# Kernel tuning notes

Hardware: AMD Instinct MI355X
Metric: run time of the kernel (lower is better)

The kernel has to match this reference:

```python
import jax, jax.numpy as jnp
import numpy as np
from jax import lax

B = 4096
D = 128
N = 81
H = 4
HD = D // H


def _conv(x, w, b, pad):
    y = lax.conv_general_dilated(x, w, (1, 1), [(pad, pad), (pad, pad)],
                                 dimension_numbers=('NCHW', 'OIHW', 'NCHW'))
    return y + b[None, :, None, None]


def _attn_mask():
    # per-head additive structural mask: same-row, same-col, same-box, global
    idx = jnp.arange(N)
    rows, cols = idx // 9, idx % 9
    boxes = rows // 3 * 3 + cols // 3
    same = lambda v: (v[:, None] == v[None, :]).astype(jnp.float32)
    return jnp.stack([same(rows), same(cols), same(boxes),
                      jnp.ones((N, N), jnp.float32)], 0)  # [4, 81, 81]


def setup_inputs():
    key = jax.random.key(0)
    ks = jax.random.split(key, 12)
    digits = jax.random.randint(ks[0], (B, 9, 9), 0, 10)
    s = jax.nn.one_hot(digits, 10, axis=1, dtype=jnp.float32)  # [B,10,9,9]

    def w(k, shape, fan):
        return jax.random.normal(k, shape, jnp.float32) / np.sqrt(fan)

    return {
        's': s,
        'c1_w': w(ks[1], (64, 10, 1, 1), 10), 'c1_b': jnp.zeros((64,)),
        'c2_w': w(ks[2], (128, 64, 3, 3), 64 * 9), 'c2_b': jnp.zeros((128,)),
        'c3_w': w(ks[3], (128, 128, 3, 3), 128 * 9), 'c3_b': jnp.zeros((128,)),
        'emb': 0.02 * jax.random.normal(ks[4], (1, N, D), jnp.float32),
        'in_w': w(ks[5], (3 * D, D), D), 'in_b': jnp.zeros((3 * D,)),
        'out_w': w(ks[6], (D, D), D), 'out_b': jnp.zeros((D,)),
        'ln_g': jnp.ones((D,)), 'ln_b': jnp.zeros((D,)),
        'l1_w': w(ks[7], (D, D), D), 'l1_b': jnp.zeros((D,)),
        'l2_w': w(ks[8], (D, D), D), 'l2_b': jnp.zeros((D,)),
        'pos_w': w(ks[9], (1, D), D), 'pos_b': jnp.zeros((1,)),
        'num_w': w(ks[10], (10, D), D), 'num_b': jnp.zeros((10,)),
    }


def reference(s, c1_w, c1_b, c2_w, c2_b, c3_w, c3_b, emb, in_w, in_b,
              out_w, out_b, ln_g, ln_b, l1_w, l1_b, l2_w, l2_b,
              pos_w, pos_b, num_w, num_b):
    # conv stem (note: no activation after c1, matching the torch code)
    x = _conv(s, c1_w, c1_b, 0)
    x = jax.nn.silu(_conv(x, c2_w, c2_b, 1))
    x = jax.nn.silu(_conv(x, c3_w, c3_b, 1))
    x = x.reshape(B, D, N).transpose(0, 2, 1) + emb  # [B,81,128]

    # MHA with per-head additive structural mask, no residual
    qkv = x @ in_w.T + in_b
    q, k, v = jnp.split(qkv, 3, axis=-1)
    heads = lambda t: t.reshape(B, N, H, HD).transpose(0, 2, 1, 3)
    q, k, v = heads(q), heads(k), heads(v)
    scores = jnp.einsum('bhqd,bhkd->bhqk', q, k) / np.sqrt(HD) + _attn_mask()[None]
    a = jax.nn.softmax(scores, axis=-1)          # [B,4,81,81]
    asc = a.mean(axis=1)                          # averaged attn weights
    ctx = jnp.einsum('bhqk,bhkd->bhqd', a, v).transpose(0, 2, 1, 3).reshape(B, N, D)
    x = ctx @ out_w.T + out_b

    # LayerNorm
    mu = x.mean(-1, keepdims=True)
    var = ((x - mu) ** 2).mean(-1, keepdims=True)
    x = (x - mu) / jnp.sqrt(var + 1e-5) * ln_g + ln_b

    x = jax.nn.silu(x @ l1_w.T + l1_b)
    x = jax.nn.silu(x @ l2_w.T + l2_b)

    # position head with masked softmax over empty cells
    pos_logits = (x @ pos_w.T + pos_b)[..., 0]    # [B,81]
    given = (s.argmax(1) != 0).reshape(B, N)
    pos_logits = jnp.where(given, -1e9, pos_logits)
    k1, k2 = jax.random.split(jax.random.key(42))
    pos = jax.random.categorical(k1, pos_logits)  # [B] int

    # number head at sampled position, digit 0 masked out
    num_logits = x @ num_w.T + num_b              # [B,81,10]
    o = jnp.take_along_axis(num_logits, pos[:, None, None], axis=1)[:, 0, :]
    o = o.at[:, 0].set(-jnp.inf)
    num = jax.random.categorical(k2, o)
    return pos, num, asc
```

## Files before the change

kernel.cpp:

```cpp
#include <hip/hip_runtime.h>
#include <stdint.h>
#include <math.h>


#define NB 4096

typedef unsigned short u16;
typedef _Float16 f16x8 __attribute__((ext_vector_type(8)));
typedef float f32x4 __attribute__((ext_vector_type(4)));

__device__ __forceinline__ float silu_f(float v) {
  return v / (1.0f + expf(-v));
}

__device__ __forceinline__ float4 zero4() { return make_float4(0.f,0.f,0.f,0.f); }

__device__ __forceinline__ void fma4b(float4& a, const float s, const float4 x) {
  a.x = fmaf(s, x.x, a.x); a.y = fmaf(s, x.y, a.y);
  a.z = fmaf(s, x.z, a.z); a.w = fmaf(s, x.w, a.w);
}

__device__ __forceinline__ void dacc(float& a, const float4 w, const float4 x) {
  a = fmaf(w.x, x.x, a); a = fmaf(w.y, x.y, a);
  a = fmaf(w.z, x.z, a); a = fmaf(w.w, x.w, a);
}

__device__ __forceinline__ void splitu(float v, u16& h, u16& l) {
  _Float16 hf = (_Float16)v;
  _Float16 lf = (_Float16)((v - (float)hf) * 2048.0f);
  union { _Float16 f; u16 u; } a, b;
  a.f = hf; b.f = lf;
  h = a.u; l = b.u;
}

__device__ __forceinline__ void tf_round(uint32_t& x0, uint32_t& x1, int r) {
  x0 += x1;
  x1 = (x1 << r) | (x1 >> (32 - r));
  x1 ^= x0;
}

__device__ __forceinline__ void threefry2x32(uint32_t k0, uint32_t k1,
                                             uint32_t x0, uint32_t x1,
                                             uint32_t& o0, uint32_t& o1) {
  uint32_t k2 = k0 ^ k1 ^ 0x1BD11BDAu;
  x0 += k0; x1 += k1;
  tf_round(x0,x1,13); tf_round(x0,x1,15); tf_round(x0,x1,26); tf_round(x0,x1,6);
  x0 += k1; x1 += k2 + 1u;
  tf_round(x0,x1,17); tf_round(x0,x1,29); tf_round(x0,x1,16); tf_round(x0,x1,24);
  x0 += k2; x1 += k0 + 2u;
  tf_round(x0,x1,13); tf_round(x0,x1,15); tf_round(x0,x1,26); tf_round(x0,x1,6);
  x0 += k0; x1 += k1 + 3u;
  tf_round(x0,x1,17); tf_round(x0,x1,29); tf_round(x0,x1,16); tf_round(x0,x1,24);
  x0 += k1; x1 += k2 + 4u;
  tf_round(x0,x1,13); tf_round(x0,x1,15); tf_round(x0,x1,26); tf_round(x0,x1,6);
  x0 += k2; x1 += k0 + 5u;
  o0 = x0; o1 = x1;
}

__device__ __forceinline__ void jax_split42(uint32_t& k1a, uint32_t& k1b,
                                            uint32_t& k2a, uint32_t& k2b) {
  threefry2x32(0u, 42u, 0u, 0u, k1a, k1b);
  threefry2x32(0u, 42u, 0u, 1u, k2a, k2b);
}

__device__ __forceinline__ uint32_t jax_randbits(uint32_t ka, uint32_t kb,
                                                 uint32_t i) {
  uint32_t o0, o1;
  threefry2x32(ka, kb, 0u, i, o0, o1);
  return o0 ^ o1;
}

__device__ __forceinline__ float jax_gumbel_bits(uint32_t bits) {
  float f = __uint_as_float((bits >> 9) | 0x3f800000u) - 1.0f;
  const float tiny = 1.17549435e-38f;
  float u = fmaxf(tiny, f + tiny);
  return -logf(-logf(u));
}

__global__ __launch_bounds__(256) void k_prep(
    const float* __restrict__ c1_w, const float* __restrict__ c1_b,
    const float* __restrict__ c2_w, const float* __restrict__ c3_w,
    const float* __restrict__ out_w, const float* __restrict__ l1_w,
    const float* __restrict__ l2_w,
    float* __restrict__ T2e, u16* __restrict__ WAh, u16* __restrict__ WAl,
    float* __restrict__ owT, float* __restrict__ l1T, float* __restrict__ l2T)
{
  int idx = blockIdx.x * 256 + threadIdx.x;
  if (idx < 9*11*128) {
    int oc = idx & 127;
    int t  = idx >> 7;
    int g  = t % 11;
    int d  = t / 11;
    float acc = 0.f;
    if (g < 10) {
      int di = d / 3, dj = d % 3;
      for (int ic = 0; ic < 64; ++ic) {
        float x1 = c1_w[ic*10 + g] + c1_b[ic];
        acc += c2_w[((oc*64 + ic)*3 + di)*3 + dj] * x1;
      }
    }
    T2e[idx] = acc;
  } else if (idx < 160128) {
    int j  = idx - 12672;
    int jj = j & 7;
    int t  = j >> 3;
    int ln = t & 63;
    int t2 = t >> 6;
    int ot = t2 & 7;
    int t3 = t2 >> 3;
    int kc = t3 & 3;
    int d  = t3 >> 2;
    int oc = ot*16 + (ln & 15);
    int ic = kc*32 + (ln >> 4)*8 + jj;
    float w = c3_w[(oc*128 + ic)*9 + d];
    u16 wh, wl;
    splitu(w, wh, wl);
    WAh[j] = wh; WAl[j] = wl;
  } else if (idx < 176512) {
    int j = idx - 160128;
    owT[j] = out_w[(j & 127)*128 + (j >> 7)];
  } else if (idx < 192896) {
    int j = idx - 176512;
    l1T[j] = l1_w[(j & 127)*128 + (j >> 7)];
  } else if (idx < 209280) {
    int j = idx - 192896;
    l2T[j] = l2_w[(j & 127)*128 + (j >> 7)];
  }
}

__global__ __launch_bounds__(256, 2) void k_stem(
    const float* __restrict__ s, const float* __restrict__ T2e,
    const float* __restrict__ c2_b,
    const u16* __restrict__ WAh, const u16* __restrict__ WAl,
    const float* __restrict__ c3_b, const float* __restrict__ emb,
    u16* __restrict__ xh, u16* __restrict__ xl, int* __restrict__ digits)
{
  __shared__ __align__(16) u16 x2h[121*128];
  __shared__ __align__(16) u16 x2l[121*128];
  __shared__ int dg[121];
  const int b   = blockIdx.x;
  const int tid = threadIdx.x;

  for (int i = tid; i < 1936; i += 256) {
    ((uint4*)x2h)[i] = make_uint4(0u,0u,0u,0u);
    ((uint4*)x2l)[i] = make_uint4(0u,0u,0u,0u);
  }
  if (tid < 121) dg[tid] = 10;
  __syncthreads();

  if (tid < 81) {
    const float* sp = s + (size_t)b*810 + tid;
    float dv = 0.f;
    #pragma unroll
    for (int c = 1; c < 10; ++c) dv += (float)c * sp[c*81];
    int d = (int)(dv + 0.5f);
    dg[(tid/9 + 1)*11 + (tid%9 + 1)] = d;
    digits[b*81 + tid] = d;
  }
  __syncthreads();

  for (int i = tid; i < 1296; i += 256) {
    const int p  = i >> 4;
    const int k8 = i & 15;
    const int r0 = p / 9, c0 = p - r0*9;
    const float4 b0 = *(const float4*)(c2_b + k8*8);
    const float4 b1 = *(const float4*)(c2_b + k8*8 + 4);
    float a0=b0.x, a1=b0.y, a2=b0.z, a3=b0.w;
    float a4=b1.x, a5=b1.y, a6=b1.z, a7=b1.w;
    #pragma unroll
    for (int d = 0; d < 9; ++d) {
      const int g = dg[(r0 + d/3)*11 + (c0 + d%3)];
      const float* tp = T2e + (size_t)(d*11 + g)*128 + k8*8;
      const float4 t0 = *(const float4*)tp;
      const float4 t1 = *(const float4*)(tp + 4);
      a0 += t0.x; a1 += t0.y; a2 += t0.z; a3 += t0.w;
      a4 += t1.x; a5 += t1.y; a6 += t1.z; a7 += t1.w;
    }
    float v[8];
    v[0]=silu_f(a0); v[1]=silu_f(a1); v[2]=silu_f(a2); v[3]=silu_f(a3);
    v[4]=silu_f(a4); v[5]=silu_f(a5); v[6]=silu_f(a6); v[7]=silu_f(a7);
    f16x8 hv, lv;
    #pragma unroll
    for (int j = 0; j < 8; ++j) {
      _Float16 h = (_Float16)v[j];
      hv[j] = h;
      lv[j] = (_Float16)((v[j] - (float)h) * 2048.0f);
    }
    const int row = (r0 + 1)*11 + (c0 + 1);
    const uint32_t bo = (uint32_t)row*256u + ((uint32_t)(k8 ^ (row & 15)) << 4);
    *(f16x8*)((char*)x2h + bo) = hv;
    *(f16x8*)((char*)x2l + bo) = lv;
  }
  __syncthreads();

  const int ln  = tid & 63;
  const int wv  = tid >> 6;
  const int lg  = ln >> 4;
  const int lr  = ln & 15;
  const int otB = (wv & 1) * 4;
  const int ntB = (wv >> 1) * 3;

  f32x4 accH[4][3];
  f32x4 accC[4][3];
  #pragma unroll
  for (int ot = 0; ot < 4; ++ot)
    #pragma unroll
    for (int nt = 0; nt < 3; ++nt) {
      accH[ot][nt] = (f32x4){0.f,0.f,0.f,0.f};
      accC[ot][nt] = (f32x4){0.f,0.f,0.f,0.f};
    }

  int pbase[3];
  #pragma unroll
  for (int nt = 0; nt < 3; ++nt) {
    const int c = (ntB + nt)*16 + lr;
    pbase[nt] = (c < 81) ? (c/9)*11 + (c%9) : 0;
  }
  const char* x2hB = (const char*)x2h;
  const char* x2lB = (const char*)x2l;

  for (int d = 0; d < 9; ++d) {
    const int off = (d/3)*11 + (d - (d/3)*3);
    int rowv[3];
    #pragma unroll
    for (int nt = 0; nt < 3; ++nt) rowv[nt] = pbase[nt] + off;
    #pragma unroll
    for (int kc = 0; kc < 4; ++kc) {
      f16x8 Bh[3], Bl[3];
      #pragma unroll
      for (int nt = 0; nt < 3; ++nt) {
        const uint32_t o = (uint32_t)rowv[nt]*256u +
            ((uint32_t)((kc*4 + lg) ^ (rowv[nt] & 15)) << 4);
        Bh[nt] = *(const f16x8*)(x2hB + o);
        Bl[nt] = *(const f16x8*)(x2lB + o);
      }
      const int abase = (((d*4 + kc)*8 + otB)*64 + ln)*8;
      f16x8 Ah[4], Al[4];
      #pragma unroll
      for (int ot = 0; ot < 4; ++ot) {
        Ah[ot] = *(const f16x8*)(WAh + abase + ot*512);
        Al[ot] = *(const f16x8*)(WAl + abase + ot*512);
      }
      #pragma unroll
      for (int ot = 0; ot < 4; ++ot)
        #pragma unroll
        for (int nt = 0; nt < 3; ++nt) {
          accH[ot][nt] = __builtin_amdgcn_mfma_f32_16x16x32_f16(
              Ah[ot], Bh[nt], accH[ot][nt], 0, 0, 0);
          accC[ot][nt] = __builtin_amdgcn_mfma_f32_16x16x32_f16(
              Ah[ot], Bl[nt], accC[ot][nt], 0, 0, 0);
          accC[ot][nt] = __builtin_amdgcn_mfma_f32_16x16x32_f16(
              Al[ot], Bh[nt], accC[ot][nt], 0, 0, 0);
        }
    }
  }

  #pragma unroll
  for (int nt = 0; nt < 3; ++nt) {
    const int cell = (ntB + nt)*16 + lr;
    if (cell < 81) {
      const size_t xoff = ((size_t)b*81 + cell)*128;
      #pragma unroll
      for (int ot = 0; ot < 4; ++ot) {
        const int oc = (otB + ot)*16 + lg*4;
        const float4 b3 = *(const float4*)(c3_b + oc);
        const float4 e  = *(const float4*)(emb + cell*128 + oc);
        const f32x4 hh = accH[ot][nt];
        const f32x4 cc = accC[ot][nt];
        float o0 = silu_f(hh[0] + cc[0]*(1.f/2048.f) + b3.x) + e.x;
        float o1 = silu_f(hh[1] + cc[1]*(1.f/2048.f) + b3.y) + e.y;
        float o2 = silu_f(hh[2] + cc[2]*(1.f/2048.f) + b3.z) + e.z;
        float o3 = silu_f(hh[3] + cc[3]*(1.f/2048.f) + b3.w) + e.w;
        ushort4 hv, lv;
        splitu(o0, hv.x, lv.x); splitu(o1, hv.y, lv.y);
        splitu(o2, hv.z, lv.z); splitu(o3, hv.w, lv.w);
        *(ushort4*)(xh + xoff + oc) = hv;
        *(ushort4*)(xl + xoff + oc) = lv;
      }
    }
  }
}

#define ATTN_LDS_BYTES 141568

__global__ __launch_bounds__(512, 1) void k_attn(
    const u16* __restrict__ xhg, const u16* __restrict__ xlg,
    const float* __restrict__ in_w, const float* __restrict__ in_b,
    float* __restrict__ ctxg, float* __restrict__ asc)
{
  extern __shared__ char smc[];
  char*  XH   = smc;
  char*  XL   = smc + 24576;
  char*  QK   = smc + 49152;
  char*  VTH  = smc + 73728;
  char*  VTL  = smc + 81920;
  float* SC   = (float*)(smc + 90112);
  char*  PH   = smc + 90112;
  char*  PL   = smc + 114688;
  float* RINV = (float*)(smc + 140800);
  uint32_t* RCB = (uint32_t*)(smc + 141184);

  const int b   = blockIdx.x;
  const int tid = threadIdx.x;
  const int ln  = tid & 63;
  const int wv  = tid >> 6;
  const int lg  = ln >> 4;
  const int lr  = ln & 15;

  if (tid < 96) {
    const int r = tid/9, c = tid - r*9;
    const int bx = (r/3)*3 + c/3;
    RCB[tid] = (uint32_t)r | ((uint32_t)c << 8) | ((uint32_t)bx << 16);
  }
  {
    const u16* gx = xhg + (size_t)b*81*128;
    const u16* gl = xlg + (size_t)b*81*128;
    for (int i = tid; i < 1296; i += 512) {
      const int n = i >> 4, k8 = i & 15;
      const uint4 hv = *(const uint4*)(gx + n*128 + k8*8);
      const uint4 lv = *(const uint4*)(gl + n*128 + k8*8);
      const uint32_t bo = (uint32_t)n*256u + ((uint32_t)(k8 ^ (n & 15)) << 4);
      *(uint4*)(XH + bo) = hv;
      *(uint4*)(XL + bo) = lv;
    }
    for (int i = tid; i < 480; i += 512) {
      char* base = (i < 240) ? XH : XL;
      const int j = (i < 240) ? i : (i - 240);
      *(uint4*)(base + 81*256 + j*16) = make_uint4(0u,0u,0u,0u);
    }
  }

  float ascR[16];
  #pragma unroll
  for (int i = 0; i < 16; ++i) ascR[i] = 0.f;

  __syncthreads();

  for (int h = 0; h < 4; ++h) {
    if (wv < 6) {
      const int part = wv >> 1;
      const int sub  = wv & 1;
      const int rowbase = part*128 + h*32 + sub*16;
      f32x4 accH[6], accC[6];
      #pragma unroll
      for (int nt = 0; nt < 6; ++nt) {
        accH[nt] = (f32x4){0.f,0.f,0.f,0.f};
        accC[nt] = (f32x4){0.f,0.f,0.f,0.f};
      }
      for (int kc = 0; kc < 4; ++kc) {
        const float* wp = in_w + (size_t)(rowbase + lr)*128 + kc*32 + lg*8;
        f16x8 Ah, Al;
        #pragma unroll
        for (int j = 0; j < 8; ++j) {
          const float w = wp[j];
          const _Float16 hf = (_Float16)w;
          Ah[j] = hf;
          Al[j] = (_Float16)((w - (float)hf) * 2048.0f);
        }
        #pragma unroll
        for (int nt = 0; nt < 6; ++nt) {
          const int row = nt*16 + lr;
          const uint32_t o = (uint32_t)row*256u +
              ((uint32_t)((kc*4 + lg) ^ (row & 15)) << 4);
          const f16x8 Bh = *(const f16x8*)(XH + o);
          const f16x8 Bl = *(const f16x8*)(XL + o);
          accH[nt] = __builtin_amdgcn_mfma_f32_16x16x32_f16(Ah, Bh, accH[nt], 0,0,0);
          accC[nt] = __builtin_amdgcn_mfma_f32_16x16x32_f16(Ah, Bl, accC[nt], 0,0,0);
          accC[nt] = __builtin_amdgcn_mfma_f32_16x16x32_f16(Al, Bh, accC[nt], 0,0,0);
        }
      }
      const float4 bia = *(const float4*)(in_b + rowbase + lg*4);
      #pragma unroll
      for (int nt = 0; nt < 6; ++nt) {
        const int cell = nt*16 + lr;
        float v0 = accH[nt][0] + accC[nt][0]*(1.f/2048.f) + bia.x;
        float v1 = accH[nt][1] + accC[nt][1]*(1.f/2048.f) + bia.y;
        float v2 = accH[nt][2] + accC[nt][2]*(1.f/2048.f) + bia.z;
        float v3 = accH[nt][3] + accC[nt][3]*(1.f/2048.f) + bia.w;
        if (part < 2) {
          ushort4 hw, lw;
          splitu(v0, hw.x, lw.x); splitu(v1, hw.y, lw.y);
          splitu(v2, hw.z, lw.z); splitu(v3, hw.w, lw.w);
          const int sflat = part*4 + sub*2 + (lg >> 1);
          const int byo   = (lg & 1)*8;
          const uint32_t adH = (uint32_t)cell*256u +
              ((uint32_t)(sflat ^ (cell & 15)) << 4) + byo;
          const uint32_t adL = (uint32_t)cell*256u +
              ((uint32_t)((8 + sflat) ^ (cell & 15)) << 4) + byo;
          *(ushort4*)(QK + adH) = hw;
          *(ushort4*)(QK + adL) = lw;
        } else {
          float vv[4] = {v0, v1, v2, v3};
          #pragma unroll
          for (int r = 0; r < 4; ++r) {
            const int hd = sub*16 + lg*4 + r;
            u16 hh, llv;
            splitu(vv[r], hh, llv);
            const uint32_t ad = (uint32_t)hd*256u +
                ((uint32_t)((cell >> 3) ^ (hd & 15)) << 4) + (cell & 7)*2;
            *(u16*)(VTH + ad) = hh;
            *(u16*)(VTL + ad) = llv;
          }
        }
      }
    }
    __syncthreads();

    {
      const uint32_t mb = (h==0) ? 0xFFu : (h==1) ? 0xFF00u
                        : (h==2) ? 0xFF0000u : 0u;
      const int t0 = (wv*36) >> 3, t1 = ((wv + 1)*36) >> 3;
      for (int t = t0; t < t1; ++t) {
        const int qt = t/6, nt = t - (t/6)*6;
        const int ra = qt*16 + lr;
        const f16x8 Qh = *(const f16x8*)(QK + (uint32_t)ra*256u +
            ((uint32_t)(lg ^ (ra & 15)) << 4));
        const f16x8 Ql = *(const f16x8*)(QK + (uint32_t)ra*256u +
            ((uint32_t)((8 + lg) ^ (ra & 15)) << 4));
        const int rb = nt*16 + lr;
        const f16x8 Kh = *(const f16x8*)(QK + (uint32_t)rb*256u +
            ((uint32_t)((4 + lg) ^ (rb & 15)) << 4));
        const f16x8 Kl = *(const f16x8*)(QK + (uint32_t)rb*256u +
            ((uint32_t)((12 + lg) ^ (rb & 15)) << 4));
        f32x4 aH = (f32x4){0.f,0.f,0.f,0.f};
        f32x4 aC = (f32x4){0.f,0.f,0.f,0.f};
        aH = __builtin_amdgcn_mfma_f32_16x16x32_f16(Qh, Kh, aH, 0,0,0);
        aC = __builtin_amdgcn_mfma_f32_16x16x32_f16(Qh, Kl, aC, 0,0,0);
        aC = __builtin_amdgcn_mfma_f32_16x16x32_f16(Ql, Kh, aC, 0,0,0);
        const int kcell = nt*16 + lr;
        const uint32_t kk = RCB[kcell];
        #pragma unroll
        for (int r = 0; r < 4; ++r) {
          const int q = qt*16 + lg*4 + r;
          const uint32_t qq = RCB[q];
          const float msk = (((qq ^ kk) & mb) == 0u) ? 1.f : 0.f;
          SC[q*132 + kcell] =
              (aH[r] + aC[r]*(1.f/2048.f)) * 0.17677669529663687f + msk;
        }
      }
    }
    __syncthreads();

    if (tid < 324) {
      const int row = tid >> 2, sub = tid & 3;
      float* sr = SC + row*132;
      const int kb = sub*24;
      const int ke = (sub == 3) ? 81 : kb + 24;
      float m = -1e30f;
      for (int k = kb; k < ke; ++k) m = fmaxf(m, sr[k]);
      m = fmaxf(m, __shfl_xor(m, 1));
      m = fmaxf(m, __shfl_xor(m, 2));
      float ss = 0.f;
      for (int k = kb; k < ke; ++k) {
        const float e = __expf(sr[k] - m);
        sr[k] = e;
        ss += e;
      }
      if (sub == 3) {
        #pragma unroll
        for (int k = 81; k < 96; ++k) sr[k] = 0.f;
      }
      ss += __shfl_xor(ss, 1);
      ss += __shfl_xor(ss, 2);
      if (sub == 0) RINV[row] = 1.0f / ss;
    }
    __syncthreads();

    float pa[2][8];
    #pragma unroll
    for (int i = 0; i < 2; ++i) {
      const int idx = tid + i*512;
      if (idx < 972) {
        const int q = idx / 12, k8 = idx - q*12;
        const float rv = RINV[q];
        const float* sp = SC + q*132 + k8*8;
        const float4 p0 = *(const float4*)sp;
        const float4 p1 = *(const float4*)(sp + 4);
        pa[i][0] = p0.x*rv; pa[i][1] = p0.y*rv;
        pa[i][2] = p0.z*rv; pa[i][3] = p0.w*rv;
        pa[i][4] = p1.x*rv; pa[i][5] = p1.y*rv;
        pa[i][6] = p1.z*rv; pa[i][7] = p1.w*rv;
        #pragma unroll
        for (int j = 0; j < 8; ++j) ascR[i*8 + j] += pa[i][j];
      }
    }
    __syncthreads();
    #pragma unroll
    for (int i = 0; i < 2; ++i) {
      const int idx = tid + i*512;
      if (idx < 972) {
        const int q = idx / 12, k8 = idx - q*12;
        union { u16 u[8]; uint4 v; } hw, lw;
        #pragma unroll
        for (int j = 0; j < 8; ++j) splitu(pa[i][j], hw.u[j], lw.u[j]);
        const uint32_t ad = (uint32_t)q*256u +
            ((uint32_t)(k8 ^ (q & 15)) << 4);
        *(uint4*)(PH + ad) = hw.v;
        *(uint4*)(PL + ad) = lw.v;
      }
    }
    __syncthreads();

    for (int t = wv; t < 12; t += 8) {
      const int ot = t/6, nt = t - (t/6)*6;
      f32x4 aH = (f32x4){0.f,0.f,0.f,0.f};
      f32x4 aC = (f32x4){0.f,0.f,0.f,0.f};
      #pragma unroll
      for (int kc = 0; kc < 3; ++kc) {
        const int ra = ot*16 + lr;
        const uint32_t oa = (uint32_t)ra*256u +
            ((uint32_t)((kc*4 + lg) ^ (ra & 15)) << 4);
        const f16x8 Vh = *(const f16x8*)(VTH + oa);
        const f16x8 Vl = *(const f16x8*)(VTL + oa);
        const int rb = nt*16 + lr;
        const uint32_t ob = (uint32_t)rb*256u +
            ((uint32_t)((kc*4 + lg) ^ (rb & 15)) << 4);
        const f16x8 Pf  = *(const f16x8*)(PH + ob);
        const f16x8 Pl2 = *(const f16x8*)(PL + ob);
        aH = __builtin_amdgcn_mfma_f32_16x16x32_f16(Vh, Pf,  aH, 0,0,0);
        aC = __builtin_amdgcn_mfma_f32_16x16x32_f16(Vh, Pl2, aC, 0,0,0);
        aC = __builtin_amdgcn_mfma_f32_16x16x32_f16(Vl, Pf,  aC, 0,0,0);
      }
      const int cell = nt*16 + lr;
      if (cell < 81) {
        float* cb = ctxg + ((size_t)b*128 + h*32 + ot*16 + lg*4)*81 + cell;
        #pragma unroll
        for (int r = 0; r < 4; ++r)
          cb[(size_t)r*81] = aH[r] + aC[r]*(1.f/2048.f);
      }
    }
    __syncthreads();
  }

  #pragma unroll
  for (int i = 0; i < 2; ++i) {
    const int idx = tid + i*512;
    if (idx < 972) {
      const int q = idx / 12, k8 = idx - q*12;
      #pragma unroll
      for (int j = 0; j < 8; ++j) {
        const int k = k8*8 + j;
        if (k < 81) asc[(size_t)b*6561 + q*81 + k] = 0.25f * ascR[i*8 + j];
      }
    }
  }
}

__global__ __launch_bounds__(256) void k_post(
    const float* __restrict__ ctxg,
    const float* __restrict__ owT,  const float* __restrict__ out_b,
    const float* __restrict__ ln_g, const float* __restrict__ ln_b,
    const float* __restrict__ l1T,  const float* __restrict__ l1_b,
    const float* __restrict__ l2T,  const float* __restrict__ l2_b,
    const float* __restrict__ pos_w, const float* __restrict__ pos_b,
    const float* __restrict__ num_w, const float* __restrict__ num_b,
    const int* __restrict__ digits,  float* __restrict__ dout)
{
  __shared__ float yT[128*84];
  __shared__ float red[243];
  __shared__ float mu[81], rstd[81];
  __shared__ float vals[81];
  __shared__ int   posIdx;
  const int b   = blockIdx.x;
  const int tid = threadIdx.x;
  const int ocg = tid >> 3;
  const int ng  = tid & 7;

  {
    const float* cb = ctxg + (size_t)b*128*81;
    for (int i = tid; i < 128*81; i += 256) {
      int k = i / 81, n = i - k*81;
      yT[k*84 + n] = cb[i];
    }
    for (int i = tid; i < 128*3; i += 256) {
      int k = i / 3, c = i - k*3;
      yT[k*84 + 81 + c] = 0.f;
    }
  }
  __syncthreads();

  {
    float4 acc[4][3];
    #pragma unroll
    for (int c = 0; c < 4; ++c)
      { acc[c][0]=zero4(); acc[c][1]=zero4(); acc[c][2]=zero4(); }
    if (ng < 7) {
      #pragma unroll 2
      for (int k = 0; k < 128; ++k) {
        const float4 wv = *(const float4*)(owT + k*128 + ocg*4);
        const float* yr = yT + k*84 + ng*12;
        float4 x0 = *(const float4*)(yr);
        float4 x1 = *(const float4*)(yr + 4);
        float4 x2 = *(const float4*)(yr + 8);
        fma4b(acc[0][0], wv.x, x0); fma4b(acc[0][1], wv.x, x1); fma4b(acc[0][2], wv.x, x2);
        fma4b(acc[1][0], wv.y, x0); fma4b(acc[1][1], wv.y, x1); fma4b(acc[1][2], wv.y, x2);
        fma4b(acc[2][0], wv.z, x0); fma4b(acc[2][1], wv.z, x1); fma4b(acc[2][2], wv.z, x2);
        fma4b(acc[3][0], wv.w, x0); fma4b(acc[3][1], wv.w, x1); fma4b(acc[3][2], wv.w, x2);
      }
    }
    __syncthreads();
    if (ng < 7) {
      #pragma unroll
      for (int c = 0; c < 4; ++c) {
        const float bv = out_b[ocg*4 + c];
        #pragma unroll
        for (int t = 0; t < 3; ++t) {
          float4 o = acc[c][t];
          o.x += bv; o.y += bv; o.z += bv; o.w += bv;
          *(float4*)(yT + (ocg*4 + c)*84 + ng*12 + t*4) = o;
        }
      }
    }
  }
  __syncthreads();

  if (tid < 243) {
    const int n = tid/3, j = tid - (tid/3)*3;
    float ssum = 0.f;
    for (int c = 0; c < 43; ++c) {
      int k = j*43 + c;
      if (k < 128) ssum += yT[k*84 + n];
    }
    red[tid] = ssum;
  }
  __syncthreads();
  if (tid < 81)
    mu[tid] = (red[tid*3] + red[tid*3+1] + red[tid*3+2]) * (1.0f/128.0f);
  __syncthreads();
  if (tid < 243) {
    const int n = tid/3, j = tid - (tid/3)*3;
    const float m = mu[n];
    float ssum = 0.f;
    for (int c = 0; c < 43; ++c) {
      int k = j*43 + c;
      if (k < 128) { float d = yT[k*84 + n] - m; ssum += d*d; }
    }
    red[tid] = ssum;
  }
  __syncthreads();
  if (tid < 81) {
    float v = (red[tid*3] + red[tid*3+1] + red[tid*3+2]) * (1.0f/128.0f);
    rstd[tid] = 1.0f / sqrtf(v + 1e-5f);
  }
  __syncthreads();
  for (int i = tid; i < 128*81; i += 256) {
    const int k = i / 81, n = i - k*81;
    yT[k*84 + n] = (yT[k*84 + n] - mu[n]) * rstd[n] * ln_g[k] + ln_b[k];
  }
  __syncthreads();

  {
    float4 acc[4][3];
    #pragma unroll
    for (int c = 0; c < 4; ++c)
      { acc[c][0]=zero4(); acc[c][1]=zero4(); acc[c][2]=zero4(); }
    if (ng < 7) {
      #pragma unroll 2
      for (int k = 0; k < 128; ++k) {
        const float4 wv = *(const float4*)(l1T + k*128 + ocg*4);
        const float* yr = yT + k*84 + ng*12;
        float4 x0 = *(const float4*)(yr);
        float4 x1 = *(const float4*)(yr + 4);
        float4 x2 = *(const float4*)(yr + 8);
        fma4b(acc[0][0], wv.x, x0); fma4b(acc[0][1], wv.x, x1); fma4b(acc[0][2], wv.x, x2);
        fma4b(acc[1][0], wv.y, x0); fma4b(acc[1][1], wv.y, x1); fma4b(acc[1][2], wv.y, x2);
        fma4b(acc[2][0], wv.z, x0); fma4b(acc[2][1], wv.z, x1); fma4b(acc[2][2], wv.z, x2);
        fma4b(acc[3][0], wv.w, x0); fma4b(acc[3][1], wv.w, x1); fma4b(acc[3][2], wv.w, x2);
      }
    }
    __syncthreads();
    if (ng < 7) {
      #pragma unroll
      for (int c = 0; c < 4; ++c) {
        const float bv = l1_b[ocg*4 + c];
        #pragma unroll
        for (int t = 0; t < 3; ++t) {
          float4 o = acc[c][t];
          o.x = silu_f(o.x + bv); o.y = silu_f(o.y + bv);
          o.z = silu_f(o.z + bv); o.w = silu_f(o.w + bv);
          *(float4*)(yT + (ocg*4 + c)*84 + ng*12 + t*4) = o;
        }
      }
    }
  }
  __syncthreads();

  {
    float4 acc[4][3];
    #pragma unroll
    for (int c = 0; c < 4; ++c)
      { acc[c][0]=zero4(); acc[c][1]=zero4(); acc[c][2]=zero4(); }
    if (ng < 7) {
      #pragma unroll 2
      for (int k = 0; k < 128; ++k) {
        const float4 wv = *(const float4*)(l2T + k*128 + ocg*4);
        const float* yr = yT + k*84 + ng*12;
        float4 x0 = *(const float4*)(yr);
        float4 x1 = *(const float4*)(yr + 4);
        float4 x2 = *(const float4*)(yr + 8);
        fma4b(acc[0][0], wv.x, x0); fma4b(acc[0][1], wv.x, x1); fma4b(acc[0][2], wv.x, x2);
        fma4b(acc[1][0], wv.y, x0); fma4b(acc[1][1], wv.y, x1); fma4b(acc[1][2], wv.y, x2);
        fma4b(acc[2][0], wv.z, x0); fma4b(acc[2][1], wv.z, x1); fma4b(acc[2][2], wv.z, x2);
        fma4b(acc[3][0], wv.w, x0); fma4b(acc[3][1], wv.w, x1); fma4b(acc[3][2], wv.w, x2);
      }
    }
    __syncthreads();
    if (ng < 7) {
      #pragma unroll
      for (int c = 0; c < 4; ++c) {
        const float bv = l2_b[ocg*4 + c];
        #pragma unroll
        for (int t = 0; t < 3; ++t) {
          float4 o = acc[c][t];
          o.x = silu_f(o.x + bv); o.y = silu_f(o.y + bv);
          o.z = silu_f(o.z + bv); o.w = silu_f(o.w + bv);
          *(float4*)(yT + (ocg*4 + c)*84 + ng*12 + t*4) = o;
        }
      }
    }
  }
  __syncthreads();

  uint32_t k1a, k1b, k2a, k2b;
  jax_split42(k1a, k1b, k2a, k2b);

  if (tid < 243) {
    const int n = tid/3, j = tid - (tid/3)*3;
    float ssum = 0.f;
    for (int c = 0; c < 43; ++c) {
      int k = j*43 + c;
      if (k < 128) ssum += yT[k*84 + n] * pos_w[k];
    }
    red[tid] = ssum;
  }
  __syncthreads();
  if (tid < 81) {
    float acc = red[tid*3] + red[tid*3+1] + red[tid*3+2] + pos_b[0];
    if (digits[b*81 + tid] != 0) acc = -1e9f;
    uint32_t bits = jax_randbits(k1a, k1b, (uint32_t)(b*81 + tid));
    vals[tid] = acc + jax_gumbel_bits(bits);
  }
  __syncthreads();
  if (tid == 0) {
    float best = vals[0]; int bi = 0;
    for (int n = 1; n < 81; ++n)
      if (vals[n] > best) { best = vals[n]; bi = n; }
    posIdx = bi;
    dout[b] = (float)bi;
  }
  __syncthreads();
  const int pos = posIdx;

  if (tid < 80) {
    const int d = tid >> 3, j = tid & 7;
    float ssum = 0.f;
    #pragma unroll
    for (int c = 0; c < 16; ++c) {
      int k = j*16 + c;
      ssum += yT[k*84 + pos] * num_w[d*128 + k];
    }
    red[tid] = ssum;
  }
  __syncthreads();
  if (tid < 10) {
    float acc = num_b[tid];
    #pragma unroll
    for (int j = 0; j < 8; ++j) acc += red[tid*8 + j];
    if (tid == 0) acc = -INFINITY;
    uint32_t bits = jax_randbits(k2a, k2b, (uint32_t)(b*10 + tid));
    vals[tid] = acc + jax_gumbel_bits(bits);
  }
  __syncthreads();
  if (tid == 0) {
    float best = vals[0]; int bi = 0;
    for (int d = 1; d < 10; ++d)
      if (vals[d] > best) { best = vals[d]; bi = d; }
    dout[NB + b] = (float)bi;
  }
}

extern "C" void kernel_launch(void* const* d_in, const int* in_sizes, int n_in,
                              void* d_out, int out_size, void* d_ws, size_t ws_size,
                              hipStream_t stream) {
  const float* s     = (const float*)d_in[0];
  const float* c1_w  = (const float*)d_in[1];
  const float* c1_b  = (const float*)d_in[2];
  const float* c2_w  = (const float*)d_in[3];
  const float* c2_b  = (const float*)d_in[4];
  const float* c3_w  = (const float*)d_in[5];
  const float* c3_b  = (const float*)d_in[6];
  const float* emb   = (const float*)d_in[7];
  const float* in_w  = (const float*)d_in[8];
  const float* in_b  = (const float*)d_in[9];
  const float* out_w = (const float*)d_in[10];
  const float* out_b = (const float*)d_in[11];
  const float* ln_g  = (const float*)d_in[12];
  const float* ln_b  = (const float*)d_in[13];
  const float* l1_w  = (const float*)d_in[14];
  const float* l1_b  = (const float*)d_in[15];
  const float* l2_w  = (const float*)d_in[16];
  const float* l2_b  = (const float*)d_in[17];
  const float* pos_w = (const float*)d_in[18];
  const float* pos_b = (const float*)d_in[19];
  const float* num_w = (const float*)d_in[20];
  const float* num_b = (const float*)d_in[21];

  float* ws     = (float*)d_ws;
  float* T2e    = ws;
  u16*   WAh    = (u16*)(ws + 12672);
  u16*   WAl    = (u16*)(ws + 86400);
  float* owT    = ws + 160128;
  float* l1T    = ws + 176512;
  float* l2T    = ws + 192896;
  int*   digits = (int*)(ws + 209280);
  u16*   xh     = (u16*)(ws + 541056);
  u16*   xl     = (u16*)(ws + 21774720);
  float* ctxg   = ws + 43008384;

  float* dout = (float*)d_out;
  float* asc  = dout + 2*NB;

  hipFuncSetAttribute((const void*)k_attn,
                      hipFuncAttributeMaxDynamicSharedMemorySize,
                      ATTN_LDS_BYTES);

  k_prep<<<dim3(818), dim3(256), 0, stream>>>(
      c1_w, c1_b, c2_w, c3_w, out_w, l1_w, l2_w,
      T2e, WAh, WAl, owT, l1T, l2T);
  k_stem<<<dim3(NB), dim3(256), 0, stream>>>(
      s, T2e, c2_b, WAh, WAl, c3_b, emb, xh, xl, digits);
  k_attn<<<dim3(NB), dim3(512), ATTN_LDS_BYTES, stream>>>(
      xh, xl, in_w, in_b, ctxg, asc);
  k_post<<<dim3(NB), dim3(256), 0, stream>>>(
      ctxg, owT, out_b, ln_g, ln_b, l1T, l1_b, l2T, l2_b,
      pos_w, pos_b, num_w, num_b, digits, dout);
}
```

Measured before the change: 1.690 ms.

## Move post-attention GEMMs and LayerNorm onto split-fp16 MFMA with register-resident epilogues

Rewrites k_post so the three 128x128 linear layers use 16x16x32 f16 MFMA with a hi/lo split-precision scheme, replacing the scalar FP32 FMA loops. Weights are pre-split and pre-swizzled into MFMA fragment order in k_prep. The attention kernel now writes ctx as cell-major hi/lo fp16 halves, which the post kernel loads into swizzled LDS. LayerNorm, bias, SiLU and the position-head dot product are done in registers using wave shuffles. This removes the slow FP32 CUDA-core GEMMs at the cost of 512 threads with one block per CU and larger LDS use, and it relies on the hi/lo split to keep accuracy.

```diff
diff --git a/kernel.cpp b/kernel.cpp
--- a/kernel.cpp
+++ b/kernel.cpp
@@ -11,18 +11,6 @@
 
 __device__ __forceinline__ float silu_f(float v) {
   return v / (1.0f + expf(-v));
-}
-
-__device__ __forceinline__ float4 zero4() { return make_float4(0.f,0.f,0.f,0.f); }
-
-__device__ __forceinline__ void fma4b(float4& a, const float s, const float4 x) {
-  a.x = fmaf(s, x.x, a.x); a.y = fmaf(s, x.y, a.y);
-  a.z = fmaf(s, x.z, a.z); a.w = fmaf(s, x.w, a.w);
-}
-
-__device__ __forceinline__ void dacc(float& a, const float4 w, const float4 x) {
-  a = fmaf(w.x, x.x, a); a = fmaf(w.y, x.y, a);
-  a = fmaf(w.z, x.z, a); a = fmaf(w.w, x.w, a);
 }
 
 __device__ __forceinline__ void splitu(float v, u16& h, u16& l) {
@@ -31,6 +19,12 @@
   union { _Float16 f; u16 u; } a, b;
   a.f = hf; b.f = lf;
   h = a.u; l = b.u;
+}
+
+__device__ __forceinline__ float joinu(u16 h, u16 l) {
+  union { u16 u; _Float16 f; } a, b;
+  a.u = h; b.u = l;
+  return (float)a.f + (float)b.f * (1.f/2048.f);
 }
 
 __device__ __forceinline__ void tf_round(uint32_t& x0, uint32_t& x1, int r) {
@@ -83,7 +77,7 @@
     const float* __restrict__ out_w, const float* __restrict__ l1_w,
     const float* __restrict__ l2_w,
     float* __restrict__ T2e, u16* __restrict__ WAh, u16* __restrict__ WAl,
-    float* __restrict__ owT, float* __restrict__ l1T, float* __restrict__ l2T)
+    u16* __restrict__ WOh, u16* __restrict__ W1h, u16* __restrict__ W2h)
 {
   int idx = blockIdx.x * 256 + threadIdx.x;
   if (idx < 9*11*128) {
@@ -116,15 +110,23 @@
     u16 wh, wl;
     splitu(w, wh, wl);
     WAh[j] = wh; WAl[j] = wl;
-  } else if (idx < 176512) {
+  } else if (idx < 209280) {
     int j = idx - 160128;
-    owT[j] = out_w[(j & 127)*128 + (j >> 7)];
-  } else if (idx < 192896) {
-    int j = idx - 176512;
-    l1T[j] = l1_w[(j & 127)*128 + (j >> 7)];
-  } else if (idx < 209280) {
-    int j = idx - 192896;
-    l2T[j] = l2_w[(j & 127)*128 + (j >> 7)];
+    int mi = j >> 14;
+    int jr = j & 16383;
+    int jj = jr & 7;
+    int t  = jr >> 3;
+    int ln = t & 63;
+    int t2 = t >> 6;
+    int ot = t2 & 7;
+    int kc = t2 >> 3;
+    int oc = ot*16 + (ln & 15);
+    int k  = kc*32 + (ln >> 4)*8 + jj;
+    const float* W = (mi == 0) ? out_w : (mi == 1) ? l1_w : l2_w;
+    u16* Dh = (mi == 0) ? WOh : (mi == 1) ? W1h : W2h;
+    u16 wh, wl;
+    splitu(W[oc*128 + k], wh, wl);
+    Dh[jr] = wh; Dh[16384 + jr] = wl;
   }
 }
 
@@ -286,7 +288,7 @@
 __global__ __launch_bounds__(512, 1) void k_attn(
     const u16* __restrict__ xhg, const u16* __restrict__ xlg,
     const float* __restrict__ in_w, const float* __restrict__ in_b,
-    float* __restrict__ ctxg, float* __restrict__ asc)
+    u16* __restrict__ ctxh, u16* __restrict__ ctxl, float* __restrict__ asc)
 {
   extern __shared__ char smc[];
   char*  XH   = smc;
@@ -523,10 +525,16 @@
       }
       const int cell = nt*16 + lr;
       if (cell < 81) {
-        float* cb = ctxg + ((size_t)b*128 + h*32 + ot*16 + lg*4)*81 + cell;
-        #pragma unroll
-        for (int r = 0; r < 4; ++r)
-          cb[(size_t)r*81] = aH[r] + aC[r]*(1.f/2048.f);
+        const size_t co = ((size_t)b*81 + cell)*128 + h*32 + ot*16 + lg*4;
+        ushort4 hw, lw;
+        float r0 = aH[0] + aC[0]*(1.f/2048.f);
+        float r1 = aH[1] + aC[1]*(1.f/2048.f);
+        float r2 = aH[2] + aC[2]*(1.f/2048.f);
+        float r3 = aH[3] + aC[3]*(1.f/2048.f);
+        splitu(r0, hw.x, lw.x); splitu(r1, hw.y, lw.y);
+        splitu(r2, hw.z, lw.z); splitu(r3, hw.w, lw.w);
+        *(ushort4*)(ctxh + co) = hw;
+        *(ushort4*)(ctxl + co) = lw;
       }
     }
     __syncthreads();
@@ -546,177 +554,193 @@
   }
 }
 
-__global__ __launch_bounds__(256) void k_post(
-    const float* __restrict__ ctxg,
-    const float* __restrict__ owT,  const float* __restrict__ out_b,
+#define POST_LDS_BYTES 105664
+
+__global__ __launch_bounds__(512, 1) void k_post(
+    const u16* __restrict__ ctxh, const u16* __restrict__ ctxl,
+    const u16* __restrict__ WOh,  const float* __restrict__ out_b,
     const float* __restrict__ ln_g, const float* __restrict__ ln_b,
-    const float* __restrict__ l1T,  const float* __restrict__ l1_b,
-    const float* __restrict__ l2T,  const float* __restrict__ l2_b,
+    const u16* __restrict__ W1h,  const float* __restrict__ l1_b,
+    const u16* __restrict__ W2h,  const float* __restrict__ l2_b,
     const float* __restrict__ pos_w, const float* __restrict__ pos_b,
     const float* __restrict__ num_w, const float* __restrict__ num_b,
     const int* __restrict__ digits,  float* __restrict__ dout)
 {
-  __shared__ float yT[128*84];
-  __shared__ float red[243];
-  __shared__ float mu[81], rstd[81];
-  __shared__ float vals[81];
-  __shared__ int   posIdx;
+  extern __shared__ char smc[];
+  char*  YH   = smc;
+  char*  YL   = smc + 24576;
+  char*  ZH   = smc + 49152;
+  char*  ZL   = smc + 73728;
+  float* red1 = (float*)(smc + 98304);
+  float* red2 = (float*)(smc + 101376);
+  float* mu   = (float*)(smc + 104448);
+  float* rstd = (float*)(smc + 104832);
+  float* vals = (float*)(smc + 105216);
+  int*   posi = (int*)(smc + 105600);
+
   const int b   = blockIdx.x;
   const int tid = threadIdx.x;
-  const int ocg = tid >> 3;
-  const int ng  = tid & 7;
+  const int ln  = tid & 63;
+  const int wv  = tid >> 6;
+  const int lg  = ln >> 4;
+  const int lr  = ln & 15;
+  const int ocb = wv*16 + lg*4;
 
   {
-    const float* cb = ctxg + (size_t)b*128*81;
-    for (int i = tid; i < 128*81; i += 256) {
-      int k = i / 81, n = i - k*81;
-      yT[k*84 + n] = cb[i];
-    }
-    for (int i = tid; i < 128*3; i += 256) {
-      int k = i / 3, c = i - k*3;
-      yT[k*84 + 81 + c] = 0.f;
-    }
-  }
-  __syncthreads();
-
+    const u16* gh = ctxh + (size_t)b*81*128;
+    const u16* gl = ctxl + (size_t)b*81*128;
+    for (int i = tid; i < 1296; i += 512) {
+      const int n = i >> 4, k8 = i & 15;
+      const uint4 hv = *(const uint4*)(gh + n*128 + k8*8);
+      const uint4 lv = *(const uint4*)(gl + n*128 + k8*8);
+      const uint32_t bo = (uint32_t)n*256u + ((uint32_t)(k8 ^ (n & 15)) << 4);
+      *(uint4*)(YH + bo) = hv;
+      *(uint4*)(YL + bo) = lv;
+    }
+    for (int i = tid; i < 480; i += 512) {
+      char* base = (i < 240) ? YH : YL;
+      const int j = (i < 240) ? i : (i - 240);
+      *(uint4*)(base + 81*256 + j*16) = make_uint4(0u,0u,0u,0u);
+    }
+  }
+  __syncthreads();
+
+  f32x4 aH[6], aC[6];
+  #define GEMM6(BH, BL, WT)                                               \
+    {                                                                     \
+      _Pragma("unroll")                                                   \
+      for (int nt = 0; nt < 6; ++nt) {                                    \
+        aH[nt] = (f32x4){0.f,0.f,0.f,0.f};                                \
+        aC[nt] = (f32x4){0.f,0.f,0.f,0.f};                                \
+      }                                                                   \
+      for (int kc = 0; kc < 4; ++kc) {                                    \
+        const int ab = ((kc*8 + wv)*64 + ln)*8;                           \
+        const f16x8 Ah = *(const f16x8*)((WT) + ab);                      \
+        const f16x8 Al = *(const f16x8*)((WT) + 16384 + ab);              \
+        _Pragma("unroll")                                                 \
+        for (int nt = 0; nt < 6; ++nt) {                                  \
+          const int row = nt*16 + lr;                                     \
+          const uint32_t o = (uint32_t)row*256u +                         \
+              ((uint32_t)((kc*4 + lg) ^ (row & 15)) << 4);                \
+          const f16x8 Bh = *(const f16x8*)((BH) + o);                     \
+          const f16x8 Bl = *(const f16x8*)((BL) + o);                     \
+          aH[nt] = __builtin_amdgcn_mfma_f32_16x16x32_f16(Ah, Bh, aH[nt], 0,0,0); \
+          aC[nt] = __builtin_amdgcn_mfma_f32_16x16x32_f16(Ah, Bl, aC[nt], 0,0,0); \
+          aC[nt] = __builtin_amdgcn_mfma_f32_16x16x32_f16(Al, Bh, aC[nt], 0,0,0); \
+        }                                                                 \
+      }                                                                   \
+    }
+
+  GEMM6(YH, YL, WOh);
+  float y[6][4];
   {
-    float4 acc[4][3];
-    #pragma unroll
-    for (int c = 0; c < 4; ++c)
-      { acc[c][0]=zero4(); acc[c][1]=zero4(); acc[c][2]=zero4(); }
-    if (ng < 7) {
-      #pragma unroll 2
-      for (int k = 0; k < 128; ++k) {
-        const float4 wv = *(const float4*)(owT + k*128 + ocg*4);
-        const float* yr = yT + k*84 + ng*12;
-        float4 x0 = *(const float4*)(yr);
-        float4 x1 = *(const float4*)(yr + 4);
-        float4 x2 = *(const float4*)(yr + 8);
-        fma4b(acc[0][0], wv.x, x0); fma4b(acc[0][1], wv.x, x1); fma4b(acc[0][2], wv.x, x2);
-        fma4b(acc[1][0], wv.y, x0); fma4b(acc[1][1], wv.y, x1); fma4b(acc[1][2], wv.y, x2);
-        fma4b(acc[2][0], wv.z, x0); fma4b(acc[2][1], wv.z, x1); fma4b(acc[2][2], wv.z, x2);
-        fma4b(acc[3][0], wv.w, x0); fma4b(acc[3][1], wv.w, x1); fma4b(acc[3][2], wv.w, x2);
-      }
-    }
-    __syncthreads();
-    if (ng < 7) {
-      #pragma unroll
-      for (int c = 0; c < 4; ++c) {
-        const float bv = out_b[ocg*4 + c];
-        #pragma unroll
-        for (int t = 0; t < 3; ++t) {
-          float4 o = acc[c][t];
-          o.x += bv; o.y += bv; o.z += bv; o.w += bv;
-          *(float4*)(yT + (ocg*4 + c)*84 + ng*12 + t*4) = o;
-        }
-      }
-    }
-  }
-  __syncthreads();
-
-  if (tid < 243) {
-    const int n = tid/3, j = tid - (tid/3)*3;
-    float ssum = 0.f;
-    for (int c = 0; c < 43; ++c) {
-      int k = j*43 + c;
-      if (k < 128) ssum += yT[k*84 + n];
-    }
-    red[tid] = ssum;
-  }
-  __syncthreads();
-  if (tid < 81)
-    mu[tid] = (red[tid*3] + red[tid*3+1] + red[tid*3+2]) * (1.0f/128.0f);
-  __syncthreads();
-  if (tid < 243) {
-    const int n = tid/3, j = tid - (tid/3)*3;
-    const float m = mu[n];
-    float ssum = 0.f;
-    for (int c = 0; c < 43; ++c) {
-      int k = j*43 + c;
-      if (k < 128) { float d = yT[k*84 + n] - m; ssum += d*d; }
-    }
-    red[tid] = ssum;
-  }
-  __syncthreads();
-  if (tid < 81) {
-    float v = (red[tid*3] + red[tid*3+1] + red[tid*3+2]) * (1.0f/128.0f);
-    rstd[tid] = 1.0f / sqrtf(v + 1e-5f);
-  }
-  __syncthreads();
-  for (int i = tid; i < 128*81; i += 256) {
-    const int k = i / 81, n = i - k*81;
-    yT[k*84 + n] = (yT[k*84 + n] - mu[n]) * rstd[n] * ln_g[k] + ln_b[k];
-  }
-  __syncthreads();
-
+    const float4 bv = *(const float4*)(out_b + ocb);
+    #pragma unroll
+    for (int nt = 0; nt < 6; ++nt) {
+      y[nt][0] = aH[nt][0] + aC[nt][0]*(1.f/2048.f) + bv.x;
+      y[nt][1] = aH[nt][1] + aC[nt][1]*(1.f/2048.f) + bv.y;
+      y[nt][2] = aH[nt][2] + aC[nt][2]*(1.f/2048.f) + bv.z;
+      y[nt][3] = aH[nt][3] + aC[nt][3]*(1.f/2048.f) + bv.w;
+    }
+  }
+
+  #pragma unroll
+  for (int nt = 0; nt < 6; ++nt) {
+    float s1 = y[nt][0] + y[nt][1] + y[nt][2] + y[nt][3];
+    s1 += __shfl_xor(s1, 16);
+    s1 += __shfl_xor(s1, 32);
+    if (ln < 16) red1[(nt*16 + lr)*8 + wv] = s1;
+  }
+  __syncthreads();
+  if (tid < 96) {
+    float s = 0.f;
+    #pragma unroll
+    for (int w = 0; w < 8; ++w) s += red1[tid*8 + w];
+    mu[tid] = s * (1.0f/128.0f);
+  }
+  __syncthreads();
+  #pragma unroll
+  for (int nt = 0; nt < 6; ++nt) {
+    const float m = mu[nt*16 + lr];
+    float d0 = y[nt][0]-m, d1 = y[nt][1]-m, d2 = y[nt][2]-m, d3 = y[nt][3]-m;
+    float s2 = d0*d0 + d1*d1 + d2*d2 + d3*d3;
+    s2 += __shfl_xor(s2, 16);
+    s2 += __shfl_xor(s2, 32);
+    if (ln < 16) red2[(nt*16 + lr)*8 + wv] = s2;
+  }
+  __syncthreads();
+  if (tid < 96) {
+    float s = 0.f;
+    #pragma unroll
+    for (int w = 0; w < 8; ++w) s += red2[tid*8 + w];
+    rstd[tid] = 1.0f / sqrtf(s * (1.0f/128.0f) + 1e-5f);
+  }
+  __syncthreads();
   {
-    float4 acc[4][3];
-    #pragma unroll
-    for (int c = 0; c < 4; ++c)
-      { acc[c][0]=zero4(); acc[c][1]=zero4(); acc[c][2]=zero4(); }
-    if (ng < 7) {
-      #pragma unroll 2
-      for (int k = 0; k < 128; ++k) {
-        const float4 wv = *(const float4*)(l1T + k*128 + ocg*4);
-        const float* yr = yT + k*84 + ng*12;
-        float4 x0 = *(const float4*)(yr);
-        float4 x1 = *(const float4*)(yr + 4);
-        float4 x2 = *(const float4*)(yr + 8);
-        fma4b(acc[0][0], wv.x, x0); fma4b(acc[0][1], wv.x, x1); fma4b(acc[0][2], wv.x, x2);
-        fma4b(acc[1][0], wv.y, x0); fma4b(acc[1][1], wv.y, x1); fma4b(acc[1][2], wv.y, x2);
-        fma4b(acc[2][0], wv.z, x0); fma4b(acc[2][1], wv.z, x1); fma4b(acc[2][2], wv.z, x2);
-        fma4b(acc[3][0], wv.w, x0); fma4b(acc[3][1], wv.w, x1); fma4b(acc[3][2], wv.w, x2);
-      }
-    }
-    __syncthreads();
-    if (ng < 7) {
-      #pragma unroll
-      for (int c = 0; c < 4; ++c) {
-        const float bv = l1_b[ocg*4 + c];
-        #pragma unroll
-        for (int t = 0; t < 3; ++t) {
-          float4 o = acc[c][t];
-          o.x = silu_f(o.x + bv); o.y = silu_f(o.y + bv);
-          o.z = silu_f(o.z + bv); o.w = silu_f(o.w + bv);
-          *(float4*)(yT + (ocg*4 + c)*84 + ng*12 + t*4) = o;
-        }
-      }
-    }
-  }
-  __syncthreads();
-
+    const float4 g  = *(const float4*)(ln_g + ocb);
+    const float4 bb = *(const float4*)(ln_b + ocb);
+    #pragma unroll
+    for (int nt = 0; nt < 6; ++nt) {
+      const int cell = nt*16 + lr;
+      const float m = mu[cell], rs = rstd[cell];
+      float z0 = (y[nt][0]-m)*rs*g.x + bb.x;
+      float z1 = (y[nt][1]-m)*rs*g.y + bb.y;
+      float z2 = (y[nt][2]-m)*rs*g.z + bb.z;
+      float z3 = (y[nt][3]-m)*rs*g.w + bb.w;
+      ushort4 hw, lw;
+      splitu(z0, hw.x, lw.x); splitu(z1, hw.y, lw.y);
+      splitu(z2, hw.z, lw.z); splitu(z3, hw.w, lw.w);
+      const uint32_t ad = (uint32_t)cell*256u +
+          ((uint32_t)((wv*2 + (lg >> 1)) ^ (cell & 15)) << 4) + (lg & 1)*8;
+      *(ushort4*)(ZH + ad) = hw;
+      *(ushort4*)(ZL + ad) = lw;
+    }
+  }
+  __syncthreads();
+
+  GEMM6(ZH, ZL, W1h);
   {
-    float4 acc[4][3];
-    #pragma unroll
-    for (int c = 0; c < 4; ++c)
-      { acc[c][0]=zero4(); acc[c][1]=zero4(); acc[c][2]=zero4(); }
-    if (ng < 7) {
-      #pragma unroll 2
-      for (int k = 0; k < 128; ++k) {
-        const float4 wv = *(const float4*)(l2T + k*128 + ocg*4);
-        const float* yr = yT + k*84 + ng*12;
-        float4 x0 = *(const float4*)(yr);
-        float4 x1 = *(const float4*)(yr + 4);
-        float4 x2 = *(const float4*)(yr + 8);
-        fma4b(acc[0][0], wv.x, x0); fma4b(acc[0][1], wv.x, x1); fma4b(acc[0][2], wv.x, x2);
-        fma4b(acc[1][0], wv.y, x0); fma4b(acc[1][1], wv.y, x1); fma4b(acc[1][2], wv.y, x2);
-        fma4b(acc[2][0], wv.z, x0); fma4b(acc[2][1], wv.z, x1); fma4b(acc[2][2], wv.z, x2);
-        fma4b(acc[3][0], wv.w, x0); fma4b(acc[3][1], wv.w, x1); fma4b(acc[3][2], wv.w, x2);
-      }
-    }
-    __syncthreads();
-    if (ng < 7) {
-      #pragma unroll
-      for (int c = 0; c < 4; ++c) {
-        const float bv = l2_b[ocg*4 + c];
-        #pragma unroll
-        for (int t = 0; t < 3; ++t) {
-          float4 o = acc[c][t];
-          o.x = silu_f(o.x + bv); o.y = silu_f(o.y + bv);
-          o.z = silu_f(o.z + bv); o.w = silu_f(o.w + bv);
-          *(float4*)(yT + (ocg*4 + c)*84 + ng*12 + t*4) = o;
-        }
-      }
+    const float4 bv = *(const float4*)(l1_b + ocb);
+    #pragma unroll
+    for (int nt = 0; nt < 6; ++nt) {
+      const int cell = nt*16 + lr;
+      float z0 = silu_f(aH[nt][0] + aC[nt][0]*(1.f/2048.f) + bv.x);
+      float z1 = silu_f(aH[nt][1] + aC[nt][1]*(1.f/2048.f) + bv.y);
+      float z2 = silu_f(aH[nt][2] + aC[nt][2]*(1.f/2048.f) + bv.z);
+      float z3 = silu_f(aH[nt][3] + aC[nt][3]*(1.f/2048.f) + bv.w);
+      ushort4 hw, lw;
+      splitu(z0, hw.x, lw.x); splitu(z1, hw.y, lw.y);
+      splitu(z2, hw.z, lw.z); splitu(z3, hw.w, lw.w);
+      const uint32_t ad = (uint32_t)cell*256u +
+          ((uint32_t)((wv*2 + (lg >> 1)) ^ (cell & 15)) << 4) + (lg & 1)*8;
+      *(ushort4*)(YH + ad) = hw;
+      *(ushort4*)(YL + ad) = lw;
+    }
+  }
+  __syncthreads();
+
+  GEMM6(YH, YL, W2h);
+  {
+    const float4 bv = *(const float4*)(l2_b + ocb);
+    const float4 pw = *(const float4*)(pos_w + ocb);
+    #pragma unroll
+    for (int nt = 0; nt < 6; ++nt) {
+      const int cell = nt*16 + lr;
+      float z0 = silu_f(aH[nt][0] + aC[nt][0]*(1.f/2048.f) + bv.x);
+      float z1 = silu_f(aH[nt][1] + aC[nt][1]*(1.f/2048.f) + bv.y);
+      float z2 = silu_f(aH[nt][2] + aC[nt][2]*(1.f/2048.f) + bv.z);
+      float z3 = silu_f(aH[nt][3] + aC[nt][3]*(1.f/2048.f) + bv.w);
+      ushort4 hw, lw;
+      splitu(z0, hw.x, lw.x); splitu(z1, hw.y, lw.y);
+      splitu(z2, hw.z, lw.z); splitu(z3, hw.w, lw.w);
+      const uint32_t ad = (uint32_t)cell*256u +
+          ((uint32_t)((wv*2 + (lg >> 1)) ^ (cell & 15)) << 4) + (lg & 1)*8;
+      *(ushort4*)(ZH + ad) = hw;
+      *(ushort4*)(ZL + ad) = lw;
+      float ps = z0*pw.x + z1*pw.y + z2*pw.z + z3*pw.w;
+      ps += __shfl_xor(ps, 16);
+      ps += __shfl_xor(ps, 32);
+      if (ln < 16) red1[cell*8 + wv] = ps;
     }
   }
   __syncthreads();
@@ -724,18 +748,10 @@
   uint32_t k1a, k1b, k2a, k2b;
   jax_split42(k1a, k1b, k2a, k2b);
 
-  if (tid < 243) {
-    const int n = tid/3, j = tid - (tid/3)*3;
-    float ssum = 0.f;
-    for (int c = 0; c < 43; ++c) {
-      int k = j*43 + c;
-      if (k < 128) ssum += yT[k*84 + n] * pos_w[k];
-    }
-    red[tid] = ssum;
-  }
-  __syncthreads();
   if (tid < 81) {
-    float acc = red[tid*3] + red[tid*3+1] + red[tid*3+2] + pos_b[0];
+    float acc = pos_b[0];
+    #pragma unroll
+    for (int w = 0; w < 8; ++w) acc += red1[tid*8 + w];
     if (digits[b*81 + tid] != 0) acc = -1e9f;
     uint32_t bits = jax_randbits(k1a, k1b, (uint32_t)(b*81 + tid));
     vals[tid] = acc + jax_gumbel_bits(bits);
@@ -745,27 +761,30 @@
     float best = vals[0]; int bi = 0;
     for (int n = 1; n < 81; ++n)
       if (vals[n] > best) { best = vals[n]; bi = n; }
-    posIdx = bi;
+    *posi = bi;
     dout[b] = (float)bi;
   }
   __syncthreads();
-  const int pos = posIdx;
+  const int pos = *posi;
 
   if (tid < 80) {
     const int d = tid >> 3, j = tid & 7;
     float ssum = 0.f;
     #pragma unroll
     for (int c = 0; c < 16; ++c) {
-      int k = j*16 + c;
-      ssum += yT[k*84 + pos] * num_w[d*128 + k];
-    }
-    red[tid] = ssum;
+      const int k = j*16 + c;
+      const uint32_t ad = (uint32_t)pos*256u +
+          ((uint32_t)((k >> 3) ^ (pos & 15)) << 4) + (k & 7)*2;
+      const float yv = joinu(*(const u16*)(ZH + ad), *(const u16*)(ZL + ad));
+      ssum += yv * num_w[d*128 + k];
+    }
+    red2[tid] = ssum;
   }
   __syncthreads();
   if (tid < 10) {
     float acc = num_b[tid];
     #pragma unroll
-    for (int j = 0; j < 8; ++j) acc += red[tid*8 + j];
+    for (int j = 0; j < 8; ++j) acc += red2[tid*8 + j];
     if (tid == 0) acc = -INFINITY;
     uint32_t bits = jax_randbits(k2a, k2b, (uint32_t)(b*10 + tid));
     vals[tid] = acc + jax_gumbel_bits(bits);
@@ -809,13 +828,14 @@
   float* T2e    = ws;
   u16*   WAh    = (u16*)(ws + 12672);
   u16*   WAl    = (u16*)(ws + 86400);
-  float* owT    = ws + 160128;
-  float* l1T    = ws + 176512;
-  float* l2T    = ws + 192896;
+  u16*   WOh    = (u16*)(ws + 160128);
+  u16*   W1h    = (u16*)(ws + 176512);
+  u16*   W2h    = (u16*)(ws + 192896);
   int*   digits = (int*)(ws + 209280);
   u16*   xh     = (u16*)(ws + 541056);
   u16*   xl     = (u16*)(ws + 21774720);
-  float* ctxg   = ws + 43008384;
+  u16*   ctxh   = (u16*)(ws + 43008384);
+  u16*   ctxl   = (u16*)(ws + 43008384 + 21233664);
 
   float* dout = (float*)d_out;
   float* asc  = dout + 2*NB;
@@ -823,15 +843,18 @@
   hipFuncSetAttribute((const void*)k_attn,
                       hipFuncAttributeMaxDynamicSharedMemorySize,
                       ATTN_LDS_BYTES);
+  hipFuncSetAttribute((const void*)k_post,
+                      hipFuncAttributeMaxDynamicSharedMemorySize,
+                      POST_LDS_BYTES);
 
   k_prep<<<dim3(818), dim3(256), 0, stream>>>(
       c1_w, c1_b, c2_w, c3_w, out_w, l1_w, l2_w,
-      T2e, WAh, WAl, owT, l1T, l2T);
+      T2e, WAh, WAl, WOh, W1h, W2h);
   k_stem<<<dim3(NB), dim3(256), 0, stream>>>(
       s, T2e, c2_b, WAh, WAl, c3_b, emb, xh, xl, digits);
   k_attn<<<dim3(NB), dim3(512), ATTN_LDS_BYTES, stream>>>(
-      xh, xl, in_w, in_b, ctxg, asc);
-  k_post<<<dim3(NB), dim3(256), 0, stream>>>(
-      ctxg, owT, out_b, ln_g, ln_b, l1T, l1_b, l2T, l2_b,
+      xh, xl, in_w, in_b, ctxh, ctxl, asc);
+  k_post<<<dim3(NB), dim3(512), POST_LDS_BYTES, stream>>>(
+      ctxh, ctxl, WOh, out_b, ln_g, ln_b, W1h, l1_b, W2h, l2_b,
       pos_w, pos_b, num_w, num_b, digits, dout);
 }
```

New measurement: 1.440 ms. 14.8% less time.
